# Kernel tuning notes

Measured on AMD Instinct MI355X. Metric: run time of the kernel, lower is better.

The kernel has to match this reference:

```python
import jax, jax.numpy as jnp
import numpy as np

N, E, D, L = 50000, 800000, 128, 2
EPS = 1e-7

def _logmap0(y):
    # Poincare ball (c=1) logmap at origin: artanh(||y||) * y / ||y||
    n = jnp.linalg.norm(y, axis=-1, keepdims=True)
    nc = jnp.clip(n, EPS, 1.0 - 1e-5)
    return jnp.arctanh(nc) * y / jnp.maximum(n, EPS)

def _expmap0(u):
    # Poincare ball (c=1) expmap at origin: tanh(||u||) * u / ||u||
    n = jnp.linalg.norm(u, axis=-1, keepdims=True)
    return jnp.tanh(n) * u / jnp.maximum(n, EPS)

def _l2norm(x):
    # F.normalize(p=2, dim=1)
    return x / jnp.maximum(jnp.linalg.norm(x, axis=1, keepdims=True), 1e-12)

def setup_inputs() -> dict:
    key = jax.random.key(0)
    ks = jax.random.split(key, 12)
    src = jax.random.randint(ks[0], (E,), 0, N)
    dst = jax.random.randint(ks[1], (E,), 0, N)
    e_emb = jax.random.normal(ks[2], (N, D), jnp.float32)
    b_emb = jax.random.normal(ks[3], (N, D), jnp.float32) * 0.1  # inside Poincare ball
    s_emb = jax.random.normal(ks[4], (N, D), jnp.float32)
    sc = 0.05
    eW = jax.random.normal(ks[5], (L, D, D), jnp.float32) * sc
    eB = jax.random.normal(ks[6], (L, D), jnp.float32) * sc
    bW = jax.random.normal(ks[7], (L, D, D), jnp.float32) * sc
    bB = jax.random.normal(ks[8], (L, D), jnp.float32) * sc
    sW = jax.random.normal(ks[9], (L, D, D), jnp.float32) * sc
    sB = jax.random.normal(ks[10], (L, D), jnp.float32) * sc
    return dict(e_emb=e_emb, b_emb=b_emb, s_emb=s_emb, eW=eW, eB=eB,
                bW=bW, bB=bB, sW=sW, sB=sB, src=src, dst=dst)

def reference(e_emb, b_emb, s_emb, eW, eB, bW, bB, sW, sB, src, dst):
    n_nodes = e_emb.shape[0]
    ones_e = jnp.ones(src.shape[0], jnp.float32)
    in_deg = jax.ops.segment_sum(ones_e, dst, num_segments=n_nodes)
    out_deg = jax.ops.segment_sum(ones_e, src, num_segments=n_nodes)
    # DGL GraphConv norm='both': D_out^{-1/2} (sum over in-neighbors) D_in^{-1/2}
    norm_out = jnp.where(out_deg > 0, out_deg ** -0.5, 0.0)[:, None]
    norm_in = jnp.where(in_deg > 0, in_deg ** -0.5, 0.0)[:, None]
    inv_in = jnp.where(in_deg > 0, 1.0 / in_deg, 0.0)[:, None]  # mean reduce

    def agg_sum(h):
        return jax.ops.segment_sum(h[src], dst, num_segments=n_nodes)

    for l in range(L):
        # Euclidean branch: GraphConv(norm='both') then LeakyReLU(0.2)
        h = agg_sum(e_emb * norm_out) * norm_in
        e_emb = jax.nn.leaky_relu(h @ eW[l].T + eB[l], negative_slope=0.2)
        # Hyperbolic branch: logmap0 -> Linear -> neighbor mean -> expmap0
        tan_b = _logmap0(b_emb) @ bW[l].T + bB[l]
        b_emb = _expmap0(agg_sum(tan_b) * inv_in)
        # Spherical branch: normalize -> Linear -> neighbor mean -> normalize
        tan_s = _l2norm(s_emb) @ sW[l].T + sB[l]
        s_emb = _l2norm(agg_sum(tan_s) * inv_in)
    return (e_emb, b_emb, s_emb)
```

## Files before the change

kernel.cpp:

```cpp
#include <hip/hip_runtime.h>
#include <math.h>

#define DD 128
#define PSTRIDE 384

typedef _Float16 half8 __attribute__((ext_vector_type(8)));
typedef _Float16 half2v __attribute__((ext_vector_type(2)));
typedef float floatx4 __attribute__((ext_vector_type(4)));

__device__ __forceinline__ float wave_sum_f(float x) {
#pragma unroll
  for (int m = 32; m >= 1; m >>= 1) x += __shfl_xor(x, m, 64);
  return x;
}
__device__ __forceinline__ float g16_sum(float x) {
#pragma unroll
  for (int m = 8; m >= 1; m >>= 1) x += __shfl_xor(x, m, 64);
  return x;
}
__device__ __forceinline__ int wave_sum_i(int x) {
#pragma unroll
  for (int m = 32; m >= 1; m >>= 1) x += __shfl_xor(x, m, 64);
  return x;
}

__global__ void degrees_kernel(const int* __restrict__ src, const int* __restrict__ dst,
                               int* __restrict__ out_deg, int* __restrict__ in_deg, int E) {
  int e = blockIdx.x * blockDim.x + threadIdx.x;
  if (e < E) {
    atomicAdd(&out_deg[src[e]], 1);
    atomicAdd(&in_deg[dst[e]], 1);
  }
}

__global__ void norms_kernel(const int* __restrict__ in_deg, const int* __restrict__ out_deg,
                             float* __restrict__ norm_in, float* __restrict__ norm_out,
                             float* __restrict__ inv_in, int N) {
  int i = blockIdx.x * blockDim.x + threadIdx.x;
  if (i < N) {
    int di = in_deg[i], dq = out_deg[i];
    norm_in[i]  = di > 0 ? 1.0f / sqrtf((float)di) : 0.0f;
    norm_out[i] = dq > 0 ? 1.0f / sqrtf((float)dq) : 0.0f;
    inv_in[i]   = di > 0 ? 1.0f / (float)di : 0.0f;
  }
}

__global__ void part_sum_kernel(const int* __restrict__ deg, int* __restrict__ part, int N) {
  __shared__ int wsum[4];
  int t = threadIdx.x, lane = t & 63, w = t >> 6;
  int i = blockIdx.x * 256 + t;
  int x = (i < N) ? deg[i] : 0;
  int s = wave_sum_i(x);
  if (lane == 0) wsum[w] = s;
  __syncthreads();
  if (t == 0) part[blockIdx.x] = wsum[0] + wsum[1] + wsum[2] + wsum[3];
}

__global__ void part_scan_kernel(int* __restrict__ part, int nb) {
  __shared__ int wsum[4];
  int t = threadIdx.x, lane = t & 63, w = t >> 6;
  int x = (t < nb) ? part[t] : 0;
  int v = x;
#pragma unroll
  for (int off = 1; off < 64; off <<= 1) {
    int y = __shfl_up(v, off, 64);
    if (lane >= off) v += y;
  }
  if (lane == 63) wsum[w] = v;
  __syncthreads();
  int base = 0;
  for (int j = 0; j < w; ++j) base += wsum[j];
  if (t < nb) part[t] = base + v - x;
}

__global__ void local_scan_kernel(const int* __restrict__ deg, const int* __restrict__ part,
                                  int* __restrict__ row_off, int N, int E) {
  __shared__ int wsum[4];
  int t = threadIdx.x, lane = t & 63, w = t >> 6;
  int i = blockIdx.x * 256 + t;
  int x = (i < N) ? deg[i] : 0;
  int v = x;
#pragma unroll
  for (int off = 1; off < 64; off <<= 1) {
    int y = __shfl_up(v, off, 64);
    if (lane >= off) v += y;
  }
  if (lane == 63) wsum[w] = v;
  __syncthreads();
  int base = 0;
  for (int j = 0; j < w; ++j) base += wsum[j];
  if (i < N) row_off[i] = part[blockIdx.x] + base + v - x;
  if (blockIdx.x == 0 && t == 0) row_off[N] = E;
}

__global__ void csr_fill_kernel(const int* __restrict__ src, const int* __restrict__ dst,
                                const float* __restrict__ norm_out,
                                const int* __restrict__ row_off, int* __restrict__ cursor,
                                int2* __restrict__ csr_sw, int E) {
  int e = blockIdx.x * blockDim.x + threadIdx.x;
  if (e < E) {
    int d = dst[e], s = src[e];
    int pos = row_off[d] + atomicAdd(&cursor[d], 1);
    csr_sw[pos] = make_int2(s, __float_as_int(norm_out[s]));
  }
}

__global__ void wcvt3_kernel(const float* __restrict__ a, const float* __restrict__ b,
                             const float* __restrict__ c, _Float16* __restrict__ o, int n) {
  int i = blockIdx.x * 256 + threadIdx.x;
  if (i < n) {
    o[i]         = (_Float16)a[i];
    o[i + n]     = (_Float16)b[i];
    o[i + 2 * n] = (_Float16)c[i];
  }
}

__global__ void pack_init_kernel(const float* __restrict__ e0, const float* __restrict__ b0,
                                 const float* __restrict__ s0, _Float16* __restrict__ P,
                                 float* __restrict__ sb, float* __restrict__ ss, int N) {
  int lane = threadIdx.x & 63;
  int v = blockIdx.x * 4 + (threadIdx.x >> 6);
  if (v >= N) return;
  size_t ri = (size_t)v * 64 + lane;
  float2 e2 = ((const float2*)e0)[ri];
  float2 b2 = ((const float2*)b0)[ri];
  float2 s2 = ((const float2*)s0)[ri];
  _Float16* Pr = P + (size_t)v * PSTRIDE + lane * 2;
  half2v he; he.x = (_Float16)e2.x; he.y = (_Float16)e2.y;
  half2v hb; hb.x = (_Float16)b2.x; hb.y = (_Float16)b2.y;
  half2v hs; hs.x = (_Float16)s2.x; hs.y = (_Float16)s2.y;
  *(half2v*)&Pr[0]   = he;
  *(half2v*)&Pr[128] = hb;
  *(half2v*)&Pr[256] = hs;
  float nb = sqrtf(wave_sum_f(b2.x * b2.x + b2.y * b2.y));
  float ns = sqrtf(wave_sum_f(s2.x * s2.x + s2.y * s2.y));
  if (lane == 0) {
    float ncb = fminf(fmaxf(nb, 1e-7f), 1.0f - 1e-5f);
    sb[v] = atanhf(ncb) / fmaxf(nb, 1e-7f);
    ss[v] = 1.0f / fmaxf(ns, 1e-12f);
  }
}

__global__ __launch_bounds__(256) void gemm3_kernel(const _Float16* __restrict__ P,
                                                    const _Float16* __restrict__ WhE,
                                                    const _Float16* __restrict__ WhB,
                                                    const _Float16* __restrict__ WhS,
                                                    const float* __restrict__ bBl,
                                                    const float* __restrict__ sBl,
                                                    const float* __restrict__ sbv,
                                                    const float* __restrict__ ssv,
                                                    _Float16* __restrict__ Qout, int N) {
  __shared__ _Float16 As[64 * 136];
  __shared__ _Float16 Ws[128 * 136];
  int part = blockIdx.y;
  const _Float16* Ain = P + part * DD;
  const _Float16* Wh = (part == 0) ? WhE : (part == 1 ? WhB : WhS);
  const float* Bb = (part == 1) ? bBl : sBl;
  const float* scv = (part == 1) ? sbv : ssv;
  _Float16* Qo = Qout + part * DD;
  int t = threadIdx.x;
  int rbase = blockIdx.x * 64;

#pragma unroll
  for (int i = 0; i < 8; ++i) {
    int idx = i * 256 + t;
    int row = idx >> 4, col = (idx & 15) * 8;
    *(half8*)&Ws[row * 136 + col] = *(const half8*)&Wh[idx * 8];
  }
  {
    int ar = t >> 2, aseg = t & 3;
    int av = rbase + ar; if (av >= N) av = N - 1;
    const _Float16* Ap = Ain + (size_t)av * PSTRIDE + aseg * 32;
    _Float16* Ad = &As[ar * 136 + aseg * 32];
    *(half8*)&Ad[0]  = *(const half8*)&Ap[0];
    *(half8*)&Ad[8]  = *(const half8*)&Ap[8];
    *(half8*)&Ad[16] = *(const half8*)&Ap[16];
    *(half8*)&Ad[24] = *(const half8*)&Ap[24];
  }
  __syncthreads();

  int lane = t & 63, w = t >> 6;
  int m = lane & 15, quad = lane >> 4;
  int c0 = w * 32;

  half8 bf[2][4];
#pragma unroll
  for (int tj = 0; tj < 2; ++tj)
#pragma unroll
    for (int kk = 0; kk < 4; ++kk)
      bf[tj][kk] = *(const half8*)&Ws[(c0 + tj * 16 + m) * 136 + kk * 32 + quad * 8];

  float bias0 = 0.f, bias1 = 0.f;
  if (part) { bias0 = Bb[c0 + m]; bias1 = Bb[c0 + 16 + m]; }

#pragma unroll
  for (int r = 0; r < 4; ++r) {
    int row0 = r * 16;
    floatx4 acc0 = {0.f, 0.f, 0.f, 0.f}, acc1 = {0.f, 0.f, 0.f, 0.f};
#pragma unroll
    for (int kk = 0; kk < 4; ++kk) {
      half8 af = *(const half8*)&As[(row0 + m) * 136 + kk * 32 + quad * 8];
      acc0 = __builtin_amdgcn_mfma_f32_16x16x32_f16(af, bf[0][kk], acc0, 0, 0, 0);
      acc1 = __builtin_amdgcn_mfma_f32_16x16x32_f16(af, bf[1][kk], acc1, 0, 0, 0);
    }
    int vrow = rbase + row0 + quad * 4;
#pragma unroll
    for (int reg = 0; reg < 4; ++reg) {
      int v = vrow + reg;
      if (v < N) {
        float x0 = acc0[reg], x1 = acc1[reg];
        if (part) { float s = scv[v]; x0 = x0 * s + bias0; x1 = x1 * s + bias1; }
        Qo[(size_t)v * PSTRIDE + c0 + m]      = (_Float16)x0;
        Qo[(size_t)v * PSTRIDE + c0 + 16 + m] = (_Float16)x1;
      }
    }
  }
}

__global__ __launch_bounds__(256) void agg_fused_kernel(
    const _Float16* __restrict__ Q, const int* __restrict__ row_off,
    const int2* __restrict__ csr_sw, const float* __restrict__ norm_in,
    const float* __restrict__ inv_in, const float* __restrict__ eBias,
    float* __restrict__ oe, float* __restrict__ ob, float* __restrict__ os,
    _Float16* __restrict__ Pnext, float* __restrict__ sb, float* __restrict__ ss,
    int N, int write_pack, int write_out) {
  int lane = threadIdx.x & 63;
  int v = blockIdx.x * 4 + (threadIdx.x >> 6);
  if (v >= N) return;
  int g = lane >> 4, q = lane & 15;
  int beg = row_off[v], end = row_off[v + 1];
  float eacc[8], bacc[8], sacc[8];
#pragma unroll
  for (int j = 0; j < 8; ++j) { eacc[j] = 0.f; bacc[j] = 0.f; sacc[j] = 0.f; }
  int i = beg;
  for (; i + 8 <= end; i += 8) {
    int2 swa = csr_sw[i + g];
    int2 swb = csr_sw[i + 4 + g];
    float wa = __int_as_float(swa.y), wb = __int_as_float(swb.y);
    const _Float16* ra = Q + (size_t)swa.x * PSTRIDE + q * 8;
    const _Float16* rb = Q + (size_t)swb.x * PSTRIDE + q * 8;
    half8 ea = *(const half8*)ra;
    half8 e2 = *(const half8*)rb;
    half8 ba = *(const half8*)(ra + 128);
    half8 b2 = *(const half8*)(rb + 128);
    half8 sa = *(const half8*)(ra + 256);
    half8 s2 = *(const half8*)(rb + 256);
#pragma unroll
    for (int j = 0; j < 8; ++j) {
      eacc[j] += wa * (float)ea[j];
      eacc[j] += wb * (float)e2[j];
      bacc[j] += (float)ba[j];
      bacc[j] += (float)b2[j];
      sacc[j] += (float)sa[j];
      sacc[j] += (float)s2[j];
    }
  }
  if (i + 4 <= end) {
    int2 sw = csr_sw[i + g];
    float wgt = __int_as_float(sw.y);
    const _Float16* rp = Q + (size_t)sw.x * PSTRIDE + q * 8;
    half8 ev = *(const half8*)rp;
    half8 bv = *(const half8*)(rp + 128);
    half8 sv = *(const half8*)(rp + 256);
#pragma unroll
    for (int j = 0; j < 8; ++j) {
      eacc[j] += wgt * (float)ev[j];
      bacc[j] += (float)bv[j];
      sacc[j] += (float)sv[j];
    }
    i += 4;
  }
  if (i + g < end) {
    int2 sw = csr_sw[i + g];
    float wgt = __int_as_float(sw.y);
    const _Float16* rp = Q + (size_t)sw.x * PSTRIDE + q * 8;
    half8 ev = *(const half8*)rp;
    half8 bv = *(const half8*)(rp + 128);
    half8 sv = *(const half8*)(rp + 256);
#pragma unroll
    for (int j = 0; j < 8; ++j) {
      eacc[j] += wgt * (float)ev[j];
      bacc[j] += (float)bv[j];
      sacc[j] += (float)sv[j];
    }
  }
#pragma unroll
  for (int j = 0; j < 8; ++j) {
    eacc[j] += __shfl_xor(eacc[j], 16, 64);
    eacc[j] += __shfl_xor(eacc[j], 32, 64);
    bacc[j] += __shfl_xor(bacc[j], 16, 64);
    bacc[j] += __shfl_xor(bacc[j], 32, 64);
    sacc[j] += __shfl_xor(sacc[j], 16, 64);
    sacc[j] += __shfl_xor(sacc[j], 32, 64);
  }
  float ni = norm_in[v], iv = inv_in[v];
  const float4* ebp = (const float4*)eBias;
  float4 eb0 = ebp[q * 2], eb1 = ebp[q * 2 + 1];
  float bias[8] = {eb0.x, eb0.y, eb0.z, eb0.w, eb1.x, eb1.y, eb1.z, eb1.w};
  float h[8], obv[8], osv[8];
  float bs2 = 0.f, ss2 = 0.f;
#pragma unroll
  for (int j = 0; j < 8; ++j) {
    float t = eacc[j] * ni + bias[j];
    h[j] = t > 0.f ? t : 0.2f * t;
    float ub = bacc[j] * iv; obv[j] = ub; bs2 += ub * ub;
    float us = sacc[j] * iv; osv[j] = us; ss2 += us * us;
  }
  float nb = sqrtf(g16_sum(bs2));
  float ns = sqrtf(g16_sum(ss2));
  float fb = tanhf(nb) / fmaxf(nb, 1e-7f);
  float fs = 1.0f / fmaxf(ns, 1e-12f);
#pragma unroll
  for (int j = 0; j < 8; ++j) { obv[j] *= fb; osv[j] *= fs; }
  if (write_out) {
    if (g == 0) {
      float4* p = (float4*)(oe + (size_t)v * DD);
      p[q * 2]     = make_float4(h[0], h[1], h[2], h[3]);
      p[q * 2 + 1] = make_float4(h[4], h[5], h[6], h[7]);
    } else if (g == 1) {
      float4* p = (float4*)(ob + (size_t)v * DD);
      p[q * 2]     = make_float4(obv[0], obv[1], obv[2], obv[3]);
      p[q * 2 + 1] = make_float4(obv[4], obv[5], obv[6], obv[7]);
    } else if (g == 2) {
      float4* p = (float4*)(os + (size_t)v * DD);
      p[q * 2]     = make_float4(osv[0], osv[1], osv[2], osv[3]);
      p[q * 2 + 1] = make_float4(osv[4], osv[5], osv[6], osv[7]);
    }
  }
  if (write_pack) {
    if (g == 3) {
      half8 he, hb, hs;
#pragma unroll
      for (int j = 0; j < 8; ++j) {
        he[j] = (_Float16)h[j];
        hb[j] = (_Float16)obv[j];
        hs[j] = (_Float16)osv[j];
      }
      _Float16* Pr = Pnext + (size_t)v * PSTRIDE + q * 8;
      *(half8*)&Pr[0]   = he;
      *(half8*)&Pr[128] = hb;
      *(half8*)&Pr[256] = hs;
    }
    if (lane == 0) {
      float mb = fb * nb;
      float ncb = fminf(fmaxf(mb, 1e-7f), 1.0f - 1e-5f);
      sb[v] = atanhf(ncb) / fmaxf(mb, 1e-7f);
      float ms = fs * ns;
      ss[v] = 1.0f / fmaxf(ms, 1e-12f);
    }
  }
}

extern "C" void kernel_launch(void* const* d_in, const int* in_sizes, int n_in,
                              void* d_out, int out_size, void* d_ws, size_t ws_size,
                              hipStream_t stream) {
  const float* e0 = (const float*)d_in[0];
  const float* b0 = (const float*)d_in[1];
  const float* s0 = (const float*)d_in[2];
  const float* eW = (const float*)d_in[3];
  const float* eB = (const float*)d_in[4];
  const float* bW = (const float*)d_in[5];
  const float* bB = (const float*)d_in[6];
  const float* sW = (const float*)d_in[7];
  const float* sB = (const float*)d_in[8];
  const int* src = (const int*)d_in[9];
  const int* dst = (const int*)d_in[10];
  int N = in_sizes[0] / DD;
  int E = in_sizes[9];
  int L = in_sizes[3] / (DD * DD);
  int LDD2 = L * DD * DD;

  char* w = (char*)d_ws;
  int* in_deg  = (int*)w; w += (size_t)N * 4;
  int* out_deg = (int*)w; w += (size_t)N * 4;
  int* cursor  = (int*)w; w += (size_t)N * 4;
  int* row_off = (int*)w; w += (size_t)(N + 4) * 4;
  int* pscan   = (int*)w; w += (size_t)1024 * 4;
  int2* csr_sw = (int2*)w; w += (size_t)E * 8;
  float* norm_in  = (float*)w; w += (size_t)N * 4;
  float* norm_out = (float*)w; w += (size_t)N * 4;
  float* inv_in   = (float*)w; w += (size_t)N * 4;
  float* sb       = (float*)w; w += (size_t)N * 4;
  float* ss       = (float*)w; w += (size_t)N * 4;
  _Float16* P     = (_Float16*)w; w += (size_t)N * PSTRIDE * 2;
  _Float16* Q     = (_Float16*)w; w += (size_t)N * PSTRIDE * 2;
  _Float16* whE   = (_Float16*)w; w += (size_t)LDD2 * 2;
  _Float16* whB   = (_Float16*)w; w += (size_t)LDD2 * 2;
  _Float16* whS   = (_Float16*)w; w += (size_t)LDD2 * 2;

  float* oe = (float*)d_out;
  float* ob = oe + (size_t)N * DD;
  float* os = ob + (size_t)N * DD;

  int PB = (N + 255) / 256;
  int AB = (N + 3) / 4;
  int GB = (N + 63) / 64;

  hipMemsetAsync(d_ws, 0, (size_t)3 * N * 4, stream);
  degrees_kernel<<<(E + 255) / 256, 256, 0, stream>>>(src, dst, out_deg, in_deg, E);
  norms_kernel<<<(N + 255) / 256, 256, 0, stream>>>(in_deg, out_deg, norm_in, norm_out, inv_in, N);
  part_sum_kernel<<<PB, 256, 0, stream>>>(in_deg, pscan, N);
  part_scan_kernel<<<1, 256, 0, stream>>>(pscan, PB);
  local_scan_kernel<<<PB, 256, 0, stream>>>(in_deg, pscan, row_off, N, E);
  csr_fill_kernel<<<(E + 255) / 256, 256, 0, stream>>>(src, dst, norm_out, row_off, cursor, csr_sw, E);
  wcvt3_kernel<<<(LDD2 + 255) / 256, 256, 0, stream>>>(eW, bW, sW, whE, LDD2);
  pack_init_kernel<<<AB, 256, 0, stream>>>(e0, b0, s0, P, sb, ss, N);

  for (int l = 0; l < L; ++l) {
    size_t lo = (size_t)l * DD * DD;
    gemm3_kernel<<<dim3(GB, 3), 256, 0, stream>>>(P, whE + lo, whB + lo, whS + lo,
                                                  bB + (size_t)l * DD, sB + (size_t)l * DD,
                                                  sb, ss, Q, N);
    agg_fused_kernel<<<AB, 256, 0, stream>>>(Q, row_off, csr_sw, norm_in, inv_in,
                                             eB + (size_t)l * DD, oe, ob, os, P, sb, ss, N,
                                             (l < L - 1) ? 1 : 0, (l == L - 1) ? 1 : 0);
  }
}
```

Before: 523.9 us.

## Fuse setup kernels, overlap CSR fill with first GEMM, fold branch scales into pack

Merges the degree counting, input packing and weight conversion into one multi-role launch, and folds the norm computation into the partial-sum kernel. The CSR fill now shares a launch with the first layer's GEMM, which runs on independent blocks. The hyperbolic and spherical scale factors are applied when P is written, so the GEMM no longer needs the per-row sb/ss arrays. The packed hyperbolic input uses the identity logmap0(expmap0(u)) = u, which is only approximate when the clip near the ball boundary is active. The GEMM also drops its LDS staging and reads A and W fragments directly from global memory, which may make those loads less efficient.

```diff
diff --git a/kernel.cpp b/kernel.cpp
--- a/kernel.cpp
+++ b/kernel.cpp
@@ -24,33 +24,65 @@
   return x;
 }
 
-__global__ void degrees_kernel(const int* __restrict__ src, const int* __restrict__ dst,
-                               int* __restrict__ out_deg, int* __restrict__ in_deg, int E) {
-  int e = blockIdx.x * blockDim.x + threadIdx.x;
-  if (e < E) {
-    atomicAdd(&out_deg[src[e]], 1);
-    atomicAdd(&in_deg[dst[e]], 1);
-  }
-}
-
-__global__ void norms_kernel(const int* __restrict__ in_deg, const int* __restrict__ out_deg,
-                             float* __restrict__ norm_in, float* __restrict__ norm_out,
-                             float* __restrict__ inv_in, int N) {
-  int i = blockIdx.x * blockDim.x + threadIdx.x;
+__global__ void setup_fused_kernel(const int* __restrict__ src, const int* __restrict__ dst,
+                                   int* __restrict__ out_deg, int* __restrict__ in_deg, int E,
+                                   const float* __restrict__ e0, const float* __restrict__ b0,
+                                   const float* __restrict__ s0, _Float16* __restrict__ P, int N,
+                                   const float* __restrict__ eW, const float* __restrict__ bW,
+                                   const float* __restrict__ sW, _Float16* __restrict__ Wh, int nW,
+                                   int DB, int AB) {
+  int bx = blockIdx.x;
+  if (bx < DB) {
+    int e = bx * 256 + threadIdx.x;
+    if (e < E) {
+      atomicAdd(&out_deg[src[e]], 1);
+      atomicAdd(&in_deg[dst[e]], 1);
+    }
+  } else if (bx < DB + AB) {
+    int lane = threadIdx.x & 63;
+    int v = (bx - DB) * 4 + (threadIdx.x >> 6);
+    if (v >= N) return;
+    size_t ri = (size_t)v * 64 + lane;
+    float2 e2 = ((const float2*)e0)[ri];
+    float2 b2 = ((const float2*)b0)[ri];
+    float2 s2 = ((const float2*)s0)[ri];
+    float nb = sqrtf(wave_sum_f(b2.x * b2.x + b2.y * b2.y));
+    float ns = sqrtf(wave_sum_f(s2.x * s2.x + s2.y * s2.y));
+    float ncb = fminf(fmaxf(nb, 1e-7f), 1.0f - 1e-5f);
+    float fb = atanhf(ncb) / fmaxf(nb, 1e-7f);
+    float fs = 1.0f / fmaxf(ns, 1e-12f);
+    _Float16* Pr = P + (size_t)v * PSTRIDE + lane * 2;
+    half2v he; he.x = (_Float16)e2.x;        he.y = (_Float16)e2.y;
+    half2v hb; hb.x = (_Float16)(b2.x * fb); hb.y = (_Float16)(b2.y * fb);
+    half2v hs; hs.x = (_Float16)(s2.x * fs); hs.y = (_Float16)(s2.y * fs);
+    *(half2v*)&Pr[0]   = he;
+    *(half2v*)&Pr[128] = hb;
+    *(half2v*)&Pr[256] = hs;
+  } else {
+    int i = (bx - DB - AB) * 256 + threadIdx.x;
+    if (i < nW) {
+      Wh[i]          = (_Float16)eW[i];
+      Wh[i + nW]     = (_Float16)bW[i];
+      Wh[i + 2 * nW] = (_Float16)sW[i];
+    }
+  }
+}
+
+__global__ void norms_psum_kernel(const int* __restrict__ in_deg, const int* __restrict__ out_deg,
+                                  float* __restrict__ norm_in, float* __restrict__ norm_out,
+                                  float* __restrict__ inv_in, int* __restrict__ part, int N) {
+  __shared__ int wsum[4];
+  int t = threadIdx.x, lane = t & 63, w = t >> 6;
+  int i = blockIdx.x * 256 + t;
+  int di = 0;
   if (i < N) {
-    int di = in_deg[i], dq = out_deg[i];
+    di = in_deg[i];
+    int dq = out_deg[i];
     norm_in[i]  = di > 0 ? 1.0f / sqrtf((float)di) : 0.0f;
     norm_out[i] = dq > 0 ? 1.0f / sqrtf((float)dq) : 0.0f;
     inv_in[i]   = di > 0 ? 1.0f / (float)di : 0.0f;
   }
-}
-
-__global__ void part_sum_kernel(const int* __restrict__ deg, int* __restrict__ part, int N) {
-  __shared__ int wsum[4];
-  int t = threadIdx.x, lane = t & 63, w = t >> 6;
-  int i = blockIdx.x * 256 + t;
-  int x = (i < N) ? deg[i] : 0;
-  int s = wave_sum_i(x);
+  int s = wave_sum_i(di);
   if (lane == 0) wsum[w] = s;
   __syncthreads();
   if (t == 0) part[blockIdx.x] = wsum[0] + wsum[1] + wsum[2] + wsum[3];
@@ -93,51 +125,69 @@
   if (blockIdx.x == 0 && t == 0) row_off[N] = E;
 }
 
-__global__ void csr_fill_kernel(const int* __restrict__ src, const int* __restrict__ dst,
-                                const float* __restrict__ norm_out,
-                                const int* __restrict__ row_off, int* __restrict__ cursor,
-                                int2* __restrict__ csr_sw, int E) {
-  int e = blockIdx.x * blockDim.x + threadIdx.x;
-  if (e < E) {
-    int d = dst[e], s = src[e];
-    int pos = row_off[d] + atomicAdd(&cursor[d], 1);
-    csr_sw[pos] = make_int2(s, __float_as_int(norm_out[s]));
-  }
-}
-
-__global__ void wcvt3_kernel(const float* __restrict__ a, const float* __restrict__ b,
-                             const float* __restrict__ c, _Float16* __restrict__ o, int n) {
-  int i = blockIdx.x * 256 + threadIdx.x;
-  if (i < n) {
-    o[i]         = (_Float16)a[i];
-    o[i + n]     = (_Float16)b[i];
-    o[i + 2 * n] = (_Float16)c[i];
-  }
-}
-
-__global__ void pack_init_kernel(const float* __restrict__ e0, const float* __restrict__ b0,
-                                 const float* __restrict__ s0, _Float16* __restrict__ P,
-                                 float* __restrict__ sb, float* __restrict__ ss, int N) {
-  int lane = threadIdx.x & 63;
-  int v = blockIdx.x * 4 + (threadIdx.x >> 6);
-  if (v >= N) return;
-  size_t ri = (size_t)v * 64 + lane;
-  float2 e2 = ((const float2*)e0)[ri];
-  float2 b2 = ((const float2*)b0)[ri];
-  float2 s2 = ((const float2*)s0)[ri];
-  _Float16* Pr = P + (size_t)v * PSTRIDE + lane * 2;
-  half2v he; he.x = (_Float16)e2.x; he.y = (_Float16)e2.y;
-  half2v hb; hb.x = (_Float16)b2.x; hb.y = (_Float16)b2.y;
-  half2v hs; hs.x = (_Float16)s2.x; hs.y = (_Float16)s2.y;
-  *(half2v*)&Pr[0]   = he;
-  *(half2v*)&Pr[128] = hb;
-  *(half2v*)&Pr[256] = hs;
-  float nb = sqrtf(wave_sum_f(b2.x * b2.x + b2.y * b2.y));
-  float ns = sqrtf(wave_sum_f(s2.x * s2.x + s2.y * s2.y));
-  if (lane == 0) {
-    float ncb = fminf(fmaxf(nb, 1e-7f), 1.0f - 1e-5f);
-    sb[v] = atanhf(ncb) / fmaxf(nb, 1e-7f);
-    ss[v] = 1.0f / fmaxf(ns, 1e-12f);
+__device__ __forceinline__ void gemm_tile(int part, int rb, const _Float16* __restrict__ P,
+                                          const _Float16* __restrict__ Wh,
+                                          const float* __restrict__ Bb,
+                                          _Float16* __restrict__ Q, int N) {
+  int t = threadIdx.x, lane = t & 63, w = t >> 6;
+  int m = lane & 15, quad = lane >> 4, c0 = w * 32;
+  int rbase = rb * 64;
+  const _Float16* Ain = P + part * DD;
+  _Float16* Qo = Q + part * DD;
+  half8 bf[2][4];
+#pragma unroll
+  for (int tj = 0; tj < 2; ++tj)
+#pragma unroll
+    for (int kk = 0; kk < 4; ++kk)
+      bf[tj][kk] = *(const half8*)&Wh[(c0 + tj * 16 + m) * DD + kk * 32 + quad * 8];
+  float bias0 = 0.f, bias1 = 0.f;
+  if (Bb) { bias0 = Bb[c0 + m]; bias1 = Bb[c0 + 16 + m]; }
+#pragma unroll
+  for (int r = 0; r < 4; ++r) {
+    int row0 = r * 16;
+    int arow = rbase + row0 + m; if (arow >= N) arow = N - 1;
+    const _Float16* Ap = Ain + (size_t)arow * PSTRIDE;
+    floatx4 acc0 = {0.f, 0.f, 0.f, 0.f}, acc1 = {0.f, 0.f, 0.f, 0.f};
+#pragma unroll
+    for (int kk = 0; kk < 4; ++kk) {
+      half8 af = *(const half8*)&Ap[kk * 32 + quad * 8];
+      acc0 = __builtin_amdgcn_mfma_f32_16x16x32_f16(af, bf[0][kk], acc0, 0, 0, 0);
+      acc1 = __builtin_amdgcn_mfma_f32_16x16x32_f16(af, bf[1][kk], acc1, 0, 0, 0);
+    }
+    int vrow = rbase + row0 + quad * 4;
+#pragma unroll
+    for (int reg = 0; reg < 4; ++reg) {
+      int v = vrow + reg;
+      if (v < N) {
+        Qo[(size_t)v * PSTRIDE + c0 + m]      = (_Float16)(acc0[reg] + bias0);
+        Qo[(size_t)v * PSTRIDE + c0 + 16 + m] = (_Float16)(acc1[reg] + bias1);
+      }
+    }
+  }
+}
+
+__global__ __launch_bounds__(256) void fill_gemm_kernel(
+    const int* __restrict__ src, const int* __restrict__ dst,
+    const float* __restrict__ norm_out, const int* __restrict__ row_off,
+    int* __restrict__ cursor, int2* __restrict__ csr_sw, int E,
+    const _Float16* __restrict__ P, const _Float16* __restrict__ WhE,
+    const _Float16* __restrict__ WhB, const _Float16* __restrict__ WhS,
+    const float* __restrict__ bBl, const float* __restrict__ sBl,
+    _Float16* __restrict__ Q, int N, int FB, int GB) {
+  int bx = blockIdx.x;
+  if (bx < FB) {
+    int e = bx * 256 + threadIdx.x;
+    if (e < E) {
+      int d = dst[e], s = src[e];
+      int pos = row_off[d] + atomicAdd(&cursor[d], 1);
+      csr_sw[pos] = make_int2(s, __float_as_int(norm_out[s]));
+    }
+  } else {
+    int gb = bx - FB;
+    int part = gb / GB, rb = gb % GB;
+    const _Float16* Wh = (part == 0) ? WhE : (part == 1 ? WhB : WhS);
+    const float* Bb = (part == 0) ? nullptr : (part == 1 ? bBl : sBl);
+    gemm_tile(part, rb, P, Wh, Bb, Q, N);
   }
 }
 
@@ -147,74 +197,11 @@
                                                     const _Float16* __restrict__ WhS,
                                                     const float* __restrict__ bBl,
                                                     const float* __restrict__ sBl,
-                                                    const float* __restrict__ sbv,
-                                                    const float* __restrict__ ssv,
-                                                    _Float16* __restrict__ Qout, int N) {
-  __shared__ _Float16 As[64 * 136];
-  __shared__ _Float16 Ws[128 * 136];
+                                                    _Float16* __restrict__ Q, int N) {
   int part = blockIdx.y;
-  const _Float16* Ain = P + part * DD;
   const _Float16* Wh = (part == 0) ? WhE : (part == 1 ? WhB : WhS);
-  const float* Bb = (part == 1) ? bBl : sBl;
-  const float* scv = (part == 1) ? sbv : ssv;
-  _Float16* Qo = Qout + part * DD;
-  int t = threadIdx.x;
-  int rbase = blockIdx.x * 64;
-
-#pragma unroll
-  for (int i = 0; i < 8; ++i) {
-    int idx = i * 256 + t;
-    int row = idx >> 4, col = (idx & 15) * 8;
-    *(half8*)&Ws[row * 136 + col] = *(const half8*)&Wh[idx * 8];
-  }
-  {
-    int ar = t >> 2, aseg = t & 3;
-    int av = rbase + ar; if (av >= N) av = N - 1;
-    const _Float16* Ap = Ain + (size_t)av * PSTRIDE + aseg * 32;
-    _Float16* Ad = &As[ar * 136 + aseg * 32];
-    *(half8*)&Ad[0]  = *(const half8*)&Ap[0];
-    *(half8*)&Ad[8]  = *(const half8*)&Ap[8];
-    *(half8*)&Ad[16] = *(const half8*)&Ap[16];
-    *(half8*)&Ad[24] = *(const half8*)&Ap[24];
-  }
-  __syncthreads();
-
-  int lane = t & 63, w = t >> 6;
-  int m = lane & 15, quad = lane >> 4;
-  int c0 = w * 32;
-
-  half8 bf[2][4];
-#pragma unroll
-  for (int tj = 0; tj < 2; ++tj)
-#pragma unroll
-    for (int kk = 0; kk < 4; ++kk)
-      bf[tj][kk] = *(const half8*)&Ws[(c0 + tj * 16 + m) * 136 + kk * 32 + quad * 8];
-
-  float bias0 = 0.f, bias1 = 0.f;
-  if (part) { bias0 = Bb[c0 + m]; bias1 = Bb[c0 + 16 + m]; }
-
-#pragma unroll
-  for (int r = 0; r < 4; ++r) {
-    int row0 = r * 16;
-    floatx4 acc0 = {0.f, 0.f, 0.f, 0.f}, acc1 = {0.f, 0.f, 0.f, 0.f};
-#pragma unroll
-    for (int kk = 0; kk < 4; ++kk) {
-      half8 af = *(const half8*)&As[(row0 + m) * 136 + kk * 32 + quad * 8];
-      acc0 = __builtin_amdgcn_mfma_f32_16x16x32_f16(af, bf[0][kk], acc0, 0, 0, 0);
-      acc1 = __builtin_amdgcn_mfma_f32_16x16x32_f16(af, bf[1][kk], acc1, 0, 0, 0);
-    }
-    int vrow = rbase + row0 + quad * 4;
-#pragma unroll
-    for (int reg = 0; reg < 4; ++reg) {
-      int v = vrow + reg;
-      if (v < N) {
-        float x0 = acc0[reg], x1 = acc1[reg];
-        if (part) { float s = scv[v]; x0 = x0 * s + bias0; x1 = x1 * s + bias1; }
-        Qo[(size_t)v * PSTRIDE + c0 + m]      = (_Float16)x0;
-        Qo[(size_t)v * PSTRIDE + c0 + 16 + m] = (_Float16)x1;
-      }
-    }
-  }
+  const float* Bb = (part == 0) ? nullptr : (part == 1 ? bBl : sBl);
+  gemm_tile(part, blockIdx.x, P, Wh, Bb, Q, N);
 }
 
 __global__ __launch_bounds__(256) void agg_fused_kernel(
@@ -222,8 +209,7 @@
     const int2* __restrict__ csr_sw, const float* __restrict__ norm_in,
     const float* __restrict__ inv_in, const float* __restrict__ eBias,
     float* __restrict__ oe, float* __restrict__ ob, float* __restrict__ os,
-    _Float16* __restrict__ Pnext, float* __restrict__ sb, float* __restrict__ ss,
-    int N, int write_pack, int write_out) {
+    _Float16* __restrict__ Pnext, int N, int write_pack, int write_out) {
   int lane = threadIdx.x & 63;
   int v = blockIdx.x * 4 + (threadIdx.x >> 6);
   if (v >= N) return;
@@ -297,34 +283,35 @@
   const float4* ebp = (const float4*)eBias;
   float4 eb0 = ebp[q * 2], eb1 = ebp[q * 2 + 1];
   float bias[8] = {eb0.x, eb0.y, eb0.z, eb0.w, eb1.x, eb1.y, eb1.z, eb1.w};
-  float h[8], obv[8], osv[8];
-  float bs2 = 0.f, ss2 = 0.f;
+  float h[8], ub[8], us[8];
+  float ss2 = 0.f;
 #pragma unroll
   for (int j = 0; j < 8; ++j) {
     float t = eacc[j] * ni + bias[j];
     h[j] = t > 0.f ? t : 0.2f * t;
-    float ub = bacc[j] * iv; obv[j] = ub; bs2 += ub * ub;
-    float us = sacc[j] * iv; osv[j] = us; ss2 += us * us;
-  }
-  float nb = sqrtf(g16_sum(bs2));
+    ub[j] = bacc[j] * iv;
+    us[j] = sacc[j] * iv; ss2 += us[j] * us[j];
+  }
   float ns = sqrtf(g16_sum(ss2));
-  float fb = tanhf(nb) / fmaxf(nb, 1e-7f);
   float fs = 1.0f / fmaxf(ns, 1e-12f);
-#pragma unroll
-  for (int j = 0; j < 8; ++j) { obv[j] *= fb; osv[j] *= fs; }
   if (write_out) {
+    float bs2 = 0.f;
+#pragma unroll
+    for (int j = 0; j < 8; ++j) bs2 += ub[j] * ub[j];
+    float nb = sqrtf(g16_sum(bs2));
+    float fb = tanhf(nb) / fmaxf(nb, 1e-7f);
     if (g == 0) {
       float4* p = (float4*)(oe + (size_t)v * DD);
       p[q * 2]     = make_float4(h[0], h[1], h[2], h[3]);
       p[q * 2 + 1] = make_float4(h[4], h[5], h[6], h[7]);
     } else if (g == 1) {
       float4* p = (float4*)(ob + (size_t)v * DD);
-      p[q * 2]     = make_float4(obv[0], obv[1], obv[2], obv[3]);
-      p[q * 2 + 1] = make_float4(obv[4], obv[5], obv[6], obv[7]);
+      p[q * 2]     = make_float4(ub[0] * fb, ub[1] * fb, ub[2] * fb, ub[3] * fb);
+      p[q * 2 + 1] = make_float4(ub[4] * fb, ub[5] * fb, ub[6] * fb, ub[7] * fb);
     } else if (g == 2) {
       float4* p = (float4*)(os + (size_t)v * DD);
-      p[q * 2]     = make_float4(osv[0], osv[1], osv[2], osv[3]);
-      p[q * 2 + 1] = make_float4(osv[4], osv[5], osv[6], osv[7]);
+      p[q * 2]     = make_float4(us[0] * fs, us[1] * fs, us[2] * fs, us[3] * fs);
+      p[q * 2 + 1] = make_float4(us[4] * fs, us[5] * fs, us[6] * fs, us[7] * fs);
     }
   }
   if (write_pack) {
@@ -333,20 +320,13 @@
 #pragma unroll
       for (int j = 0; j < 8; ++j) {
         he[j] = (_Float16)h[j];
-        hb[j] = (_Float16)obv[j];
-        hs[j] = (_Float16)osv[j];
+        hb[j] = (_Float16)ub[j];
+        hs[j] = (_Float16)(us[j] * fs);
       }
       _Float16* Pr = Pnext + (size_t)v * PSTRIDE + q * 8;
       *(half8*)&Pr[0]   = he;
       *(half8*)&Pr[128] = hb;
       *(half8*)&Pr[256] = hs;
-    }
-    if (lane == 0) {
-      float mb = fb * nb;
-      float ncb = fminf(fmaxf(mb, 1e-7f), 1.0f - 1e-5f);
-      sb[v] = atanhf(ncb) / fmaxf(mb, 1e-7f);
-      float ms = fs * ns;
-      ss[v] = 1.0f / fmaxf(ms, 1e-12f);
     }
   }
 }
@@ -380,39 +360,42 @@
   float* norm_in  = (float*)w; w += (size_t)N * 4;
   float* norm_out = (float*)w; w += (size_t)N * 4;
   float* inv_in   = (float*)w; w += (size_t)N * 4;
-  float* sb       = (float*)w; w += (size_t)N * 4;
-  float* ss       = (float*)w; w += (size_t)N * 4;
-  _Float16* P     = (_Float16*)w; w += (size_t)N * PSTRIDE * 2;
-  _Float16* Q     = (_Float16*)w; w += (size_t)N * PSTRIDE * 2;
-  _Float16* whE   = (_Float16*)w; w += (size_t)LDD2 * 2;
-  _Float16* whB   = (_Float16*)w; w += (size_t)LDD2 * 2;
-  _Float16* whS   = (_Float16*)w; w += (size_t)LDD2 * 2;
+  w = (char*)(((size_t)w + 255) & ~(size_t)255);
+  _Float16* P = (_Float16*)w; w += (size_t)N * PSTRIDE * 2;
+  _Float16* Q = (_Float16*)w; w += (size_t)N * PSTRIDE * 2;
+  _Float16* Wh = (_Float16*)w; w += (size_t)3 * LDD2 * 2;
+  _Float16* whE = Wh;
+  _Float16* whB = Wh + LDD2;
+  _Float16* whS = Wh + 2 * LDD2;
 
   float* oe = (float*)d_out;
   float* ob = oe + (size_t)N * DD;
   float* os = ob + (size_t)N * DD;
 
-  int PB = (N + 255) / 256;
+  int DB = (E + 255) / 256;
   int AB = (N + 3) / 4;
   int GB = (N + 63) / 64;
+  int WB = (LDD2 + 255) / 256;
+  int PB = (N + 255) / 256;
 
   hipMemsetAsync(d_ws, 0, (size_t)3 * N * 4, stream);
-  degrees_kernel<<<(E + 255) / 256, 256, 0, stream>>>(src, dst, out_deg, in_deg, E);
-  norms_kernel<<<(N + 255) / 256, 256, 0, stream>>>(in_deg, out_deg, norm_in, norm_out, inv_in, N);
-  part_sum_kernel<<<PB, 256, 0, stream>>>(in_deg, pscan, N);
+  setup_fused_kernel<<<DB + AB + WB, 256, 0, stream>>>(src, dst, out_deg, in_deg, E,
+                                                       e0, b0, s0, P, N,
+                                                       eW, bW, sW, Wh, LDD2, DB, AB);
+  norms_psum_kernel<<<PB, 256, 0, stream>>>(in_deg, out_deg, norm_in, norm_out, inv_in, pscan, N);
   part_scan_kernel<<<1, 256, 0, stream>>>(pscan, PB);
   local_scan_kernel<<<PB, 256, 0, stream>>>(in_deg, pscan, row_off, N, E);
-  csr_fill_kernel<<<(E + 255) / 256, 256, 0, stream>>>(src, dst, norm_out, row_off, cursor, csr_sw, E);
-  wcvt3_kernel<<<(LDD2 + 255) / 256, 256, 0, stream>>>(eW, bW, sW, whE, LDD2);
-  pack_init_kernel<<<AB, 256, 0, stream>>>(e0, b0, s0, P, sb, ss, N);
-
-  for (int l = 0; l < L; ++l) {
+  fill_gemm_kernel<<<DB + 3 * GB, 256, 0, stream>>>(src, dst, norm_out, row_off, cursor, csr_sw, E,
+                                                    P, whE, whB, whS, bB, sB, Q, N, DB, GB);
+  agg_fused_kernel<<<AB, 256, 0, stream>>>(Q, row_off, csr_sw, norm_in, inv_in, eB,
+                                           oe, ob, os, P, N,
+                                           (L > 1) ? 1 : 0, (L == 1) ? 1 : 0);
+  for (int l = 1; l < L; ++l) {
     size_t lo = (size_t)l * DD * DD;
     gemm3_kernel<<<dim3(GB, 3), 256, 0, stream>>>(P, whE + lo, whB + lo, whS + lo,
-                                                  bB + (size_t)l * DD, sB + (size_t)l * DD,
-                                                  sb, ss, Q, N);
+                                                  bB + (size_t)l * DD, sB + (size_t)l * DD, Q, N);
     agg_fused_kernel<<<AB, 256, 0, stream>>>(Q, row_off, csr_sw, norm_in, inv_in,
-                                             eB + (size_t)l * DD, oe, ob, os, P, sb, ss, N,
+                                             eB + (size_t)l * DD, oe, ob, os, P, N,
                                              (l < L - 1) ? 1 : 0, (l == L - 1) ? 1 : 0);
   }
 }
```

New measurement: 496.2 us. 5.3% less time.
